# Performance work log

Hardware: AMD Instinct MI355X
Metric: run time of the kernel (lower is better)

## Reference

```python
import jax, jax.numpy as jnp
import numpy as np

N_NODES = 50000
N_EDGES = 800000
IN_FEAT = 128
HID = 128
OUT = 10
N_GRAPHS = 128
BN_EPS = 1e-5


def setup_inputs() -> dict:
    key = jax.random.key(0)
    ks = jax.random.split(key, 16)
    inp = {
        "n_feat": jax.random.normal(ks[0], (N_NODES, IN_FEAT), dtype=jnp.float32),
        "src": jax.random.randint(ks[1], (N_EDGES,), 0, N_NODES),
        "dst": jax.random.randint(ks[2], (N_EDGES,), 0, N_NODES),
        "graph_ids": jnp.sort(jax.random.randint(ks[3], (N_NODES,), 0, N_GRAPHS)),
        # GraphConv weights (DGL layout: weight [in, out], bias [out])
        "W1": jax.random.normal(ks[4], (IN_FEAT, HID), dtype=jnp.float32) / np.sqrt(IN_FEAT),
        "b1": jnp.zeros((HID,), dtype=jnp.float32),
        "W2": jax.random.normal(ks[5], (HID, HID), dtype=jnp.float32) / np.sqrt(HID),
        "b2": jnp.zeros((HID,), dtype=jnp.float32),
        # BatchNorm1d affine params
        "gamma": jnp.ones((HID,), dtype=jnp.float32),
        "beta": jnp.zeros((HID,), dtype=jnp.float32),
        # MLP head
        "fc1_w": jax.random.normal(ks[6], (HID, HID), dtype=jnp.float32) / np.sqrt(HID),
        "fc1_b": jnp.zeros((HID,), dtype=jnp.float32),
        "fc2_w": jax.random.normal(ks[7], (HID, OUT), dtype=jnp.float32) / np.sqrt(HID),
        "fc2_b": jnp.zeros((OUT,), dtype=jnp.float32),
    }
    return inp


def _graph_conv(x, W, b, src, dst, inv_sqrt_out, inv_sqrt_in):
    # DGL GraphConv, norm='both': h = D_in^{-1/2} A D_out^{-1/2} x W + b
    h = x * inv_sqrt_out[:, None]          # [N, d_in]
    h = h @ W                              # [N, d_out] (project before gather: fewer bytes moved)
    agg = jax.ops.segment_sum(h[src], dst, num_segments=N_NODES)  # gather + scatter-add
    return agg * inv_sqrt_in[:, None] + b


def reference(n_feat, src, dst, graph_ids, W1, b1, W2, b2, gamma, beta,
              fc1_w, fc1_b, fc2_w, fc2_b):
    ones_e = jnp.ones((N_EDGES,), dtype=jnp.float32)
    deg_out = jnp.clip(jax.ops.segment_sum(ones_e, src, num_segments=N_NODES), 1.0)
    deg_in = jnp.clip(jax.ops.segment_sum(ones_e, dst, num_segments=N_NODES), 1.0)
    inv_sqrt_out = jax.lax.rsqrt(deg_out)
    inv_sqrt_in = jax.lax.rsqrt(deg_in)

    x = jax.nn.relu(_graph_conv(n_feat, W1, b1, src, dst, inv_sqrt_out, inv_sqrt_in))
    # dropout is identity in eval mode
    x = jax.nn.relu(_graph_conv(x, W2, b2, src, dst, inv_sqrt_out, inv_sqrt_in))

    # SumPooling over graphs
    embedding = jax.ops.segment_sum(x, graph_ids, num_segments=N_GRAPHS)  # [B, HID]

    # BatchNorm1d (training-mode batch stats, biased variance like torch)
    mu = jnp.mean(embedding, axis=0)
    var = jnp.mean(jnp.square(embedding - mu), axis=0)
    h = gamma * (embedding - mu) * jax.lax.rsqrt(var + BN_EPS) + beta

    h = jax.nn.relu(h @ fc1_w + fc1_b)
    logits = h @ fc2_w + fc2_b
    return embedding, jax.nn.log_softmax(logits, axis=-1)
```

## Files before the change

kernel.cpp:

```cpp
#include <hip/hip_runtime.h>
#include <hip/hip_bf16.h>
#include <math.h>

#define N_NODES 50000
#define N_EDGES 800000
#define HID 128
#define N_GRAPHS 128
#define OUTC 10
#define BN_EPS 1e-5f

#define SCAN_B 256
#define N_SCAN_BLOCKS ((N_NODES + SCAN_B - 1) / SCAN_B)

#define POOL_CHUNK 32
#define N_POOL_BLOCKS ((N_NODES + POOL_CHUNK - 1) / POOL_CHUNK)

#define HB 80
#define HWORDS (N_NODES / 2)
#define HR_B 128
#define HR_BLOCKS ((HWORDS + HR_B - 1) / HR_B)

#define EPAD 8
#define E_SRC_CAP (N_EDGES + N_NODES * EPAD)

#define LDA 136

typedef short short8 __attribute__((ext_vector_type(8)));
typedef float floatx4 __attribute__((ext_vector_type(4)));

template <typename T, typename F>
__device__ inline T bitcast(F f) {
    union { F a; T b; } u;
    u.a = f;
    return u.b;
}

__global__ __launch_bounds__(1024) void hist_part_kernel(const int* __restrict__ src,
                                                         const int* __restrict__ dst,
                                                         unsigned int* __restrict__ part,
                                                         const float* __restrict__ W1,
                                                         const float* __restrict__ W2,
                                                         unsigned short* __restrict__ Wp) {
    if (blockIdx.x == 2 * HB) {
        for (int q = threadIdx.x; q < 4096; q += 1024) {
            int wi = q >> 11;
            const float* __restrict__ W = wi ? W2 : W1;
            int t2 = q & 2047;
            int tile = t2 >> 6, lane = t2 & 63;
            int kc = tile >> 3, nt = tile & 7;
            int n = lane & 15, quad = lane >> 4;
            unsigned short v[8];
#pragma unroll
            for (int j = 0; j < 8; j++) {
                int k = kc * 32 + quad * 8 + j;
                v[j] = __hip_bfloat16_raw(__float2bfloat16(W[k * HID + nt * 16 + n])).x;
            }
            *(uint4*)&Wp[(size_t)q * 8] = *(uint4*)v;
        }
        return;
    }
    __shared__ unsigned int h[HWORDS];
    for (int i = threadIdx.x; i < HWORDS; i += 1024) h[i] = 0;
    __syncthreads();
    int half = (blockIdx.x >= HB) ? 1 : 0;
    const int* __restrict__ idx = half ? dst : src;
    int b = blockIdx.x - half * HB;
    for (int e = b * 1024 + threadIdx.x; e < N_EDGES; e += HB * 1024) {
        int v = idx[e];
        atomicAdd(&h[v >> 1], 1u << ((v & 1) << 4));
    }
    __syncthreads();
    unsigned int* __restrict__ out = part + (size_t)blockIdx.x * HWORDS;
    for (int i = threadIdx.x; i < HWORDS; i += 1024) out[i] = h[i];
}

__global__ __launch_bounds__(HR_B) void hist_reduce_kernel(unsigned int* __restrict__ part,
                                                           int* __restrict__ cnt_in,
                                                           float* __restrict__ inv_out,
                                                           float* __restrict__ inv_in,
                                                           int* __restrict__ bsum) {
    int w = blockIdx.x * HR_B + threadIdx.x;
    int padsum = 0;
    if (w < HWORDS) {
        unsigned int s = 0, d = 0;
        for (int b = 0; b < HB; b++) {
            s += part[(size_t)b * HWORDS + w];
            unsigned int c = part[(size_t)(b + HB) * HWORDS + w];
            part[(size_t)(b + HB) * HWORDS + w] = d;
            d += c;
        }
        int i0 = w * 2, i1 = i0 + 1;
        int so0 = (int)(s & 0xFFFFu), so1 = (int)(s >> 16);
        int di0 = (int)(d & 0xFFFFu), di1 = (int)(d >> 16);
        cnt_in[i0] = di0;
        cnt_in[i1] = di1;
        inv_out[i0] = rsqrtf(fmaxf((float)so0, 1.0f));
        inv_out[i1] = rsqrtf(fmaxf((float)so1, 1.0f));
        inv_in[i0] = rsqrtf(fmaxf((float)di0, 1.0f));
        inv_in[i1] = rsqrtf(fmaxf((float)di1, 1.0f));
        padsum = ((di0 + EPAD - 1) & ~(EPAD - 1)) + ((di1 + EPAD - 1) & ~(EPAD - 1));
    }
    __shared__ int red[HR_B];
    red[threadIdx.x] = padsum;
    __syncthreads();
    for (int o = HR_B / 2; o > 0; o >>= 1) {
        if (threadIdx.x < o) red[threadIdx.x] += red[threadIdx.x + o];
        __syncthreads();
    }
    if (threadIdx.x == 0) bsum[blockIdx.x] = red[0];
}

__global__ void scan_bsum_kernel(const int* __restrict__ bsum, int* __restrict__ boff) {
    __shared__ int part[SCAN_B];
    int t = threadIdx.x;
    int v = (t < N_SCAN_BLOCKS) ? bsum[t] : 0;
    part[t] = v;
    __syncthreads();
    for (int off = 1; off < SCAN_B; off <<= 1) {
        int u = (t >= off) ? part[t - off] : 0;
        __syncthreads();
        part[t] += u;
        __syncthreads();
    }
    boff[t] = part[t] - v;
}

__global__ void scan_write_kernel(const int* __restrict__ cnt, const int* __restrict__ boff,
                                  int* __restrict__ row_ptr, int* __restrict__ edge_src) {
    __shared__ int part[SCAN_B];
    int t = threadIdx.x;
    int i = blockIdx.x * SCAN_B + t;
    int raw = (i < N_NODES) ? cnt[i] : 0;
    int v = (raw + EPAD - 1) & ~(EPAD - 1);
    part[t] = v;
    __syncthreads();
    for (int off = 1; off < SCAN_B; off <<= 1) {
        int u = (t >= off) ? part[t - off] : 0;
        __syncthreads();
        part[t] += u;
        __syncthreads();
    }
    if (i < N_NODES) {
        int ex = part[t] - v + boff[blockIdx.x];
        row_ptr[i] = ex;
        for (int p = ex + raw; p < ex + v; p++) edge_src[p] = N_NODES;
        if (i == N_NODES - 1) row_ptr[N_NODES] = ex + v;
    }
}

__global__ __launch_bounds__(1024) void csr_fill_kernel(const int* __restrict__ src,
                                                        const int* __restrict__ dst,
                                                        const unsigned int* __restrict__ part,
                                                        const int* __restrict__ row_ptr,
                                                        int* __restrict__ edge_src) {
    __shared__ unsigned int loc[HWORDS];
    int b = blockIdx.x;
    const unsigned int* __restrict__ off = part + (size_t)(b + HB) * HWORDS;
    for (int i = threadIdx.x; i < HWORDS; i += 1024) loc[i] = off[i];
    __syncthreads();
    for (int e = b * 1024 + threadIdx.x; e < N_EDGES; e += HB * 1024) {
        int d = dst[e];
        unsigned int old = atomicAdd(&loc[d >> 1], 1u << ((d & 1) << 4));
        int local = (d & 1) ? (int)(old >> 16) : (int)(old & 0xFFFFu);
        edge_src[row_ptr[d] + local] = src[e];
    }
}

__global__ __launch_bounds__(256) void matmul_kernel(const float* __restrict__ X,
                                                     const float* __restrict__ scale,
                                                     const unsigned short* __restrict__ Wp,
                                                     __hip_bfloat16* __restrict__ Y) {
    __shared__ unsigned short xs[64 * LDA];
    int tid = threadIdx.x;
    int row0 = blockIdx.x * 64;

    for (int j = 0; j < 8; j++) {
        int idx4 = j * 256 + tid;
        int r = idx4 >> 5;
        int col = (idx4 & 31) * 4;
        int rg = row0 + r;
        float4 v = make_float4(0.f, 0.f, 0.f, 0.f);
        if (rg < N_NODES) {
            v = *(const float4*)&X[(size_t)rg * HID + col];
            float sc = scale[rg];
            v.x *= sc; v.y *= sc; v.z *= sc; v.w *= sc;
        }
        unsigned short o[4];
        o[0] = __hip_bfloat16_raw(__float2bfloat16(v.x)).x;
        o[1] = __hip_bfloat16_raw(__float2bfloat16(v.y)).x;
        o[2] = __hip_bfloat16_raw(__float2bfloat16(v.z)).x;
        o[3] = __hip_bfloat16_raw(__float2bfloat16(v.w)).x;
        *(ushort4*)&xs[r * LDA + col] = *(ushort4*)o;
    }
    __syncthreads();

    int wave = tid >> 6, lane = tid & 63;
    int m = lane & 15, quad = lane >> 4;
    int rowl = wave * 16;

    short8 a[4];
#pragma unroll
    for (int kc = 0; kc < 4; kc++)
        a[kc] = bitcast<short8>(*(const uint4*)&xs[(rowl + m) * LDA + kc * 32 + quad * 8]);

    floatx4 acc[8];
#pragma unroll
    for (int nt = 0; nt < 8; nt++) acc[nt] = (floatx4){0.f, 0.f, 0.f, 0.f};

#pragma unroll
    for (int nt = 0; nt < 8; nt++) {
#pragma unroll
        for (int kc = 0; kc < 4; kc++) {
            short8 bfr = bitcast<short8>(
                *(const uint4*)&Wp[((size_t)(kc * 8 + nt) * 64 + lane) * 8]);
            acc[nt] = __builtin_amdgcn_mfma_f32_16x16x32_bf16(a[kc], bfr, acc[nt], 0, 0, 0);
        }
    }

#pragma unroll
    for (int nt = 0; nt < 8; nt++) {
#pragma unroll
        for (int i = 0; i < 4; i++) {
            int rg = row0 + rowl + quad * 4 + i;
            if (rg < N_NODES + 1) {
                Y[(size_t)rg * HID + nt * 16 + m] = __float2bfloat16(acc[nt][i]);
            }
        }
    }
}

__global__ __launch_bounds__(256) void agg_kernel(const __hip_bfloat16* __restrict__ Y,
                                                  const int* __restrict__ edge_src,
                                                  const int* __restrict__ row_ptr,
                                                  const float* __restrict__ inv_in,
                                                  const float* __restrict__ bias,
                                                  float* __restrict__ Xout) {
    const uint4* __restrict__ Yq = (const uint4*)Y;
    int wave = threadIdx.x >> 6;
    int lane = threadIdx.x & 63;
    int n = blockIdx.x * 4 + wave;
    if (n >= N_NODES) return;
    int beg = row_ptr[n], end = row_ptr[n + 1];
    int esub = lane >> 4;
    int f16  = lane & 15;
    float acc[8] = {};
    for (int base = beg; base < end; base += 64) {
        int mm = min(64, end - base);
        int idx = (lane < mm) ? edge_src[base + lane] : N_NODES;
        for (int j = 0; j < mm; j += 8) {
            int s0 = __shfl(idx, j + esub);
            int s1 = __shfl(idx, j + 4 + esub);
            uint4 u0 = Yq[s0 * (HID / 8) + f16];
            uint4 u1 = Yq[s1 * (HID / 8) + f16];
            acc[0] += __uint_as_float(u0.x << 16); acc[1] += __uint_as_float(u0.x & 0xFFFF0000u);
            acc[2] += __uint_as_float(u0.y << 16); acc[3] += __uint_as_float(u0.y & 0xFFFF0000u);
            acc[4] += __uint_as_float(u0.z << 16); acc[5] += __uint_as_float(u0.z & 0xFFFF0000u);
            acc[6] += __uint_as_float(u0.w << 16); acc[7] += __uint_as_float(u0.w & 0xFFFF0000u);
            acc[0] += __uint_as_float(u1.x << 16); acc[1] += __uint_as_float(u1.x & 0xFFFF0000u);
            acc[2] += __uint_as_float(u1.y << 16); acc[3] += __uint_as_float(u1.y & 0xFFFF0000u);
            acc[4] += __uint_as_float(u1.z << 16); acc[5] += __uint_as_float(u1.z & 0xFFFF0000u);
            acc[6] += __uint_as_float(u1.w << 16); acc[7] += __uint_as_float(u1.w & 0xFFFF0000u);
        }
    }
#pragma unroll
    for (int i = 0; i < 8; i++) {
        acc[i] += __shfl_xor(acc[i], 16);
        acc[i] += __shfl_xor(acc[i], 32);
    }
    if (lane < 16) {
        float si = inv_in[n];
        int f0 = f16 * 8;
        float4 b0 = *(const float4*)&bias[f0];
        float4 b1 = *(const float4*)&bias[f0 + 4];
        float4 o0, o1;
        o0.x = fmaxf(acc[0] * si + b0.x, 0.f);
        o0.y = fmaxf(acc[1] * si + b0.y, 0.f);
        o0.z = fmaxf(acc[2] * si + b0.z, 0.f);
        o0.w = fmaxf(acc[3] * si + b0.w, 0.f);
        o1.x = fmaxf(acc[4] * si + b1.x, 0.f);
        o1.y = fmaxf(acc[5] * si + b1.y, 0.f);
        o1.z = fmaxf(acc[6] * si + b1.z, 0.f);
        o1.w = fmaxf(acc[7] * si + b1.w, 0.f);
        *(float4*)&Xout[(size_t)n * HID + f0] = o0;
        *(float4*)&Xout[(size_t)n * HID + f0 + 4] = o1;
    }
}

__global__ __launch_bounds__(64) void pool_kernel(const float* __restrict__ X,
                                                  const int* __restrict__ gid,
                                                  float* __restrict__ emb) {
    int lane = threadIdx.x;
    int n0 = blockIdx.x * POOL_CHUNK;
    int n1 = min(n0 + POOL_CHUNK, N_NODES);
    if (n0 >= N_NODES) return;
    int g_cur = gid[n0];
    float ax = 0.f, ay = 0.f;
    for (int n = n0; n < n1; n++) {
        int g = gid[n];
        if (g != g_cur) {
            atomicAdd(&emb[g_cur * HID + lane * 2], ax);
            atomicAdd(&emb[g_cur * HID + lane * 2 + 1], ay);
            ax = 0.f; ay = 0.f;
            g_cur = g;
        }
        float2 v = *(const float2*)&X[(size_t)n * HID + lane * 2];
        ax += v.x;
        ay += v.y;
    }
    atomicAdd(&emb[g_cur * HID + lane * 2], ax);
    atomicAdd(&emb[g_cur * HID + lane * 2 + 1], ay);
}

__global__ __launch_bounds__(128) void head_fused_kernel(const float* __restrict__ emb,
                                                         const float* __restrict__ gamma,
                                                         const float* __restrict__ beta,
                                                         const float* __restrict__ fc1_w,
                                                         const float* __restrict__ fc1_b,
                                                         const float* __restrict__ fc2_w,
                                                         const float* __restrict__ fc2_b,
                                                         float* __restrict__ out) {
    int r = blockIdx.x, f = threadIdx.x;
    float s = 0.f;
    for (int row = 0; row < N_GRAPHS; row++) s += emb[row * HID + f];
    float mu = s * (1.f / N_GRAPHS);
    float v = 0.f;
    for (int row = 0; row < N_GRAPHS; row++) {
        float d = emb[row * HID + f] - mu;
        v += d * d;
    }
    v *= (1.f / N_GRAPHS);
    float sc = gamma[f] * rsqrtf(v + BN_EPS);
    float sh = beta[f] - mu * sc;

    __shared__ float xr[HID];
    xr[f] = emb[r * HID + f] * sc + sh;
    __syncthreads();
    float acc = fc1_b[f];
    for (int k = 0; k < HID; k++) acc += xr[k] * fc1_w[k * HID + f];
    __shared__ float hr[HID];
    hr[f] = fmaxf(acc, 0.f);
    __syncthreads();

    __shared__ float logits[OUTC];
    __shared__ float mstat[2];
    if (f < OUTC) {
        float a = fc2_b[f];
        for (int k = 0; k < HID; k++) a += hr[k] * fc2_w[k * OUTC + f];
        logits[f] = a;
    }
    __syncthreads();
    if (f == 0) {
        float m = logits[0];
        for (int o = 1; o < OUTC; o++) m = fmaxf(m, logits[o]);
        float sum = 0.f;
        for (int o = 0; o < OUTC; o++) sum += expf(logits[o] - m);
        mstat[0] = m;
        mstat[1] = logf(sum);
    }
    __syncthreads();
    if (f < OUTC) out[r * OUTC + f] = logits[f] - mstat[0] - mstat[1];
}

extern "C" void kernel_launch(void* const* d_in, const int* in_sizes, int n_in,
                              void* d_out, int out_size, void* d_ws, size_t ws_size,
                              hipStream_t stream) {
    const float* n_feat = (const float*)d_in[0];
    const int*   src    = (const int*)d_in[1];
    const int*   dst    = (const int*)d_in[2];
    const int*   gid    = (const int*)d_in[3];
    const float* W1     = (const float*)d_in[4];
    const float* b1     = (const float*)d_in[5];
    const float* W2     = (const float*)d_in[6];
    const float* b2     = (const float*)d_in[7];
    const float* gamma  = (const float*)d_in[8];
    const float* beta   = (const float*)d_in[9];
    const float* fc1_w  = (const float*)d_in[10];
    const float* fc1_b  = (const float*)d_in[11];
    const float* fc2_w  = (const float*)d_in[12];
    const float* fc2_b  = (const float*)d_in[13];

    char* wsb = (char*)d_ws;
    size_t off = 0;
    auto alloc = [&](size_t bytes) -> void* {
        void* p = wsb + off;
        off += (bytes + 255) & ~(size_t)255;
        return p;
    };
    int*   cnt_in  = (int*)alloc((size_t)N_NODES * 4);
    int*   row_ptr = (int*)alloc((size_t)(N_NODES + 1) * 4);
    int*   e_src   = (int*)alloc((size_t)E_SRC_CAP * 4);
    float* inv_out = (float*)alloc((size_t)N_NODES * 4);
    float* inv_in  = (float*)alloc((size_t)N_NODES * 4);
    void*  ybuf    = alloc((size_t)2 * HB * HWORDS * 4);
    float* X       = (float*)alloc((size_t)N_NODES * HID * 4);
    unsigned short* Wp = (unsigned short*)alloc((size_t)2 * 32 * 64 * 8 * 2);
    int*   bsum    = (int*)alloc((size_t)SCAN_B * 4);
    int*   boff    = (int*)alloc((size_t)SCAN_B * 4);

    unsigned int*   part = (unsigned int*)ybuf;
    __hip_bfloat16* Y    = (__hip_bfloat16*)ybuf;

    float* emb_out = (float*)d_out;
    float* lsm_out = emb_out + N_GRAPHS * HID;

    hipMemsetAsync(emb_out, 0, (size_t)N_GRAPHS * HID * 4, stream);

    hist_part_kernel<<<2 * HB + 1, 1024, 0, stream>>>(src, dst, part, W1, W2, Wp);
    hist_reduce_kernel<<<HR_BLOCKS, HR_B, 0, stream>>>(part, cnt_in, inv_out, inv_in, bsum);
    scan_bsum_kernel<<<1, SCAN_B, 0, stream>>>(bsum, boff);
    scan_write_kernel<<<N_SCAN_BLOCKS, SCAN_B, 0, stream>>>(cnt_in, boff, row_ptr, e_src);
    csr_fill_kernel<<<HB, 1024, 0, stream>>>(src, dst, part, row_ptr, e_src);

    matmul_kernel<<<(N_NODES + 64) / 64, 256, 0, stream>>>(n_feat, inv_out, Wp, Y);
    agg_kernel<<<(N_NODES + 3) / 4, 256, 0, stream>>>(Y, e_src, row_ptr, inv_in, b1, X);
    matmul_kernel<<<(N_NODES + 64) / 64, 256, 0, stream>>>(X, inv_out, Wp + (size_t)32 * 64 * 8, Y);
    agg_kernel<<<(N_NODES + 3) / 4, 256, 0, stream>>>(Y, e_src, row_ptr, inv_in, b2, X);

    pool_kernel<<<N_POOL_BLOCKS, 64, 0, stream>>>(X, gid, emb_out);
    head_fused_kernel<<<N_GRAPHS, HID, 0, stream>>>(emb_out, gamma, beta, fc1_w, fc1_b,
                                                    fc2_w, fc2_b, lsm_out);
}
```

Measured before the change: 254.6 us.

## Fuse CSR-build kernels via grid barriers, emit bf16 layer-1 output, fuse pool+head

Merges the histogram, reduce, scan and CSR-fill kernels into one persistent kernel that separates its phases with atomic-counter grid barriers. It also merges the pooling and head kernels the same way, and drops the memset of the embedding. The first aggregation now applies the out-degree scale and writes bf16, so the second matmul reads half the bytes and skips conversion. This removes several launch gaps and one fp32 round trip. In exchange it relies on all blocks being co-resident for the spin barriers, which risks deadlock if they are not.

```diff
diff --git a/kernel.cpp b/kernel.cpp
--- a/kernel.cpp
+++ b/kernel.cpp
@@ -9,21 +9,18 @@
 #define OUTC 10
 #define BN_EPS 1e-5f
 
-#define SCAN_B 256
-#define N_SCAN_BLOCKS ((N_NODES + SCAN_B - 1) / SCAN_B)
-
-#define POOL_CHUNK 32
-#define N_POOL_BLOCKS ((N_NODES + POOL_CHUNK - 1) / POOL_CHUNK)
-
 #define HB 80
 #define HWORDS (N_NODES / 2)
 #define HR_B 128
-#define HR_BLOCKS ((HWORDS + HR_B - 1) / HR_B)
+#define NPRE 196
 
 #define EPAD 8
 #define E_SRC_CAP (N_EDGES + N_NODES * EPAD)
 
 #define LDA 136
+
+#define PH_BLOCKS 256
+#define PH_NODES ((N_NODES + PH_BLOCKS - 1) / PH_BLOCKS)
 
 typedef short short8 __attribute__((ext_vector_type(8)));
 typedef float floatx4 __attribute__((ext_vector_type(4)));
@@ -35,14 +32,56 @@
     return u.b;
 }
 
-__global__ __launch_bounds__(1024) void hist_part_kernel(const int* __restrict__ src,
-                                                         const int* __restrict__ dst,
-                                                         unsigned int* __restrict__ part,
-                                                         const float* __restrict__ W1,
-                                                         const float* __restrict__ W2,
-                                                         unsigned short* __restrict__ Wp) {
-    if (blockIdx.x == 2 * HB) {
-        for (int q = threadIdx.x; q < 4096; q += 1024) {
+__device__ inline unsigned short f2bf(float x) {
+    return __hip_bfloat16_raw(__float2bfloat16(x)).x;
+}
+
+__device__ inline void grid_sync(unsigned int* ctr, unsigned int nblk, bool wait) {
+    __syncthreads();
+    if (threadIdx.x == 0) {
+        __hip_atomic_fetch_add(ctr, 1u, __ATOMIC_RELEASE, __HIP_MEMORY_SCOPE_AGENT);
+        if (wait) {
+            while (__hip_atomic_load(ctr, __ATOMIC_RELAXED, __HIP_MEMORY_SCOPE_AGENT) < nblk)
+                __builtin_amdgcn_s_sleep(2);
+        }
+    }
+    __syncthreads();
+    if (wait) __threadfence();
+}
+
+__global__ __launch_bounds__(1024) void pre_kernel(const int* __restrict__ src,
+                                                   const int* __restrict__ dst,
+                                                   unsigned int* __restrict__ part,
+                                                   const float* __restrict__ W1,
+                                                   const float* __restrict__ W2,
+                                                   unsigned short* __restrict__ Wp,
+                                                   float* __restrict__ inv_out,
+                                                   float* __restrict__ inv_in,
+                                                   int* __restrict__ row_ptr,
+                                                   int* __restrict__ edge_src,
+                                                   int* __restrict__ bsum,
+                                                   float* __restrict__ emb,
+                                                   unsigned int* __restrict__ ctr) {
+    __shared__ unsigned int big[HWORDS];
+    __shared__ int cnts[2 * HR_B];
+    __shared__ int red[HR_B];
+    int b = blockIdx.x, t = threadIdx.x;
+
+    if (b < 2 * HB) {
+        for (int i = t; i < HWORDS; i += 1024) big[i] = 0;
+        __syncthreads();
+        int half = (b >= HB) ? 1 : 0;
+        const int* __restrict__ idx = half ? dst : src;
+        int bb = b - half * HB;
+        for (int e = bb * 1024 + t; e < N_EDGES; e += HB * 1024) {
+            int v = idx[e];
+            atomicAdd(&big[v >> 1], 1u << ((v & 1) << 4));
+        }
+        __syncthreads();
+        unsigned int* __restrict__ out = part + (size_t)b * HWORDS;
+        for (int i = t; i < HWORDS; i += 1024) out[i] = big[i];
+    } else if (b == 2 * HB) {
+        for (int q = t; q < 4096; q += 1024) {
             int wi = q >> 11;
             const float* __restrict__ W = wi ? W2 : W1;
             int t2 = q & 2047;
@@ -53,116 +92,130 @@
 #pragma unroll
             for (int j = 0; j < 8; j++) {
                 int k = kc * 32 + quad * 8 + j;
-                v[j] = __hip_bfloat16_raw(__float2bfloat16(W[k * HID + nt * 16 + n])).x;
+                v[j] = f2bf(W[k * HID + nt * 16 + n]);
             }
             *(uint4*)&Wp[(size_t)q * 8] = *(uint4*)v;
         }
-        return;
-    }
-    __shared__ unsigned int h[HWORDS];
-    for (int i = threadIdx.x; i < HWORDS; i += 1024) h[i] = 0;
-    __syncthreads();
-    int half = (blockIdx.x >= HB) ? 1 : 0;
-    const int* __restrict__ idx = half ? dst : src;
-    int b = blockIdx.x - half * HB;
-    for (int e = b * 1024 + threadIdx.x; e < N_EDGES; e += HB * 1024) {
-        int v = idx[e];
-        atomicAdd(&h[v >> 1], 1u << ((v & 1) << 4));
-    }
-    __syncthreads();
-    unsigned int* __restrict__ out = part + (size_t)blockIdx.x * HWORDS;
-    for (int i = threadIdx.x; i < HWORDS; i += 1024) out[i] = h[i];
-}
-
-__global__ __launch_bounds__(HR_B) void hist_reduce_kernel(unsigned int* __restrict__ part,
-                                                           int* __restrict__ cnt_in,
-                                                           float* __restrict__ inv_out,
-                                                           float* __restrict__ inv_in,
-                                                           int* __restrict__ bsum) {
-    int w = blockIdx.x * HR_B + threadIdx.x;
+    } else if (b == 2 * HB + 1) {
+        for (int i = t; i < N_GRAPHS * HID; i += 1024) emb[i] = 0.f;
+    }
+    grid_sync(ctr + 0, NPRE, true);
+
     int padsum = 0;
-    if (w < HWORDS) {
-        unsigned int s = 0, d = 0;
-        for (int b = 0; b < HB; b++) {
-            s += part[(size_t)b * HWORDS + w];
-            unsigned int c = part[(size_t)(b + HB) * HWORDS + w];
-            part[(size_t)(b + HB) * HWORDS + w] = d;
-            d += c;
-        }
-        int i0 = w * 2, i1 = i0 + 1;
-        int so0 = (int)(s & 0xFFFFu), so1 = (int)(s >> 16);
-        int di0 = (int)(d & 0xFFFFu), di1 = (int)(d >> 16);
-        cnt_in[i0] = di0;
-        cnt_in[i1] = di1;
-        inv_out[i0] = rsqrtf(fmaxf((float)so0, 1.0f));
-        inv_out[i1] = rsqrtf(fmaxf((float)so1, 1.0f));
-        inv_in[i0] = rsqrtf(fmaxf((float)di0, 1.0f));
-        inv_in[i1] = rsqrtf(fmaxf((float)di1, 1.0f));
-        padsum = ((di0 + EPAD - 1) & ~(EPAD - 1)) + ((di1 + EPAD - 1) & ~(EPAD - 1));
-    }
-    __shared__ int red[HR_B];
-    red[threadIdx.x] = padsum;
+    if (t < HR_B) {
+        int w = b * HR_B + t;
+        int di0 = 0, di1 = 0;
+        if (w < HWORDS) {
+            unsigned int s = 0, d = 0;
+#pragma unroll 10
+            for (int bb = 0; bb < HB; bb++) {
+                s += part[(size_t)bb * HWORDS + w];
+                unsigned int c = part[(size_t)(bb + HB) * HWORDS + w];
+                part[(size_t)(bb + HB) * HWORDS + w] = d;
+                d += c;
+            }
+            int i0 = w * 2, i1 = i0 + 1;
+            int so0 = (int)(s & 0xFFFFu), so1 = (int)(s >> 16);
+            di0 = (int)(d & 0xFFFFu);
+            di1 = (int)(d >> 16);
+            inv_out[i0] = rsqrtf(fmaxf((float)so0, 1.0f));
+            inv_out[i1] = rsqrtf(fmaxf((float)so1, 1.0f));
+            inv_in[i0] = rsqrtf(fmaxf((float)di0, 1.0f));
+            inv_in[i1] = rsqrtf(fmaxf((float)di1, 1.0f));
+            padsum = ((di0 + EPAD - 1) & ~(EPAD - 1)) + ((di1 + EPAD - 1) & ~(EPAD - 1));
+        }
+        cnts[2 * t] = di0;
+        cnts[2 * t + 1] = di1;
+        red[t] = padsum;
+    }
     __syncthreads();
     for (int o = HR_B / 2; o > 0; o >>= 1) {
-        if (threadIdx.x < o) red[threadIdx.x] += red[threadIdx.x + o];
-        __syncthreads();
-    }
-    if (threadIdx.x == 0) bsum[blockIdx.x] = red[0];
-}
-
-__global__ void scan_bsum_kernel(const int* __restrict__ bsum, int* __restrict__ boff) {
-    __shared__ int part[SCAN_B];
-    int t = threadIdx.x;
-    int v = (t < N_SCAN_BLOCKS) ? bsum[t] : 0;
-    part[t] = v;
-    __syncthreads();
-    for (int off = 1; off < SCAN_B; off <<= 1) {
-        int u = (t >= off) ? part[t - off] : 0;
-        __syncthreads();
-        part[t] += u;
-        __syncthreads();
-    }
-    boff[t] = part[t] - v;
-}
-
-__global__ void scan_write_kernel(const int* __restrict__ cnt, const int* __restrict__ boff,
-                                  int* __restrict__ row_ptr, int* __restrict__ edge_src) {
-    __shared__ int part[SCAN_B];
-    int t = threadIdx.x;
-    int i = blockIdx.x * SCAN_B + t;
-    int raw = (i < N_NODES) ? cnt[i] : 0;
+        if (t < o) red[t] += red[t + o];
+        __syncthreads();
+    }
+    if (t == 0) bsum[b] = red[0];
+    grid_sync(ctr + 1, NPRE, true);
+
+    int* sb = (int*)big;
+    int* sc = (int*)big + 256;
+    if (t < 256) sb[t] = (t < NPRE) ? bsum[t] : 0;
+    __syncthreads();
+    for (int off = 1; off < 256; off <<= 1) {
+        int u = (t < 256 && t >= off) ? sb[t - off] : 0;
+        __syncthreads();
+        if (t < 256) sb[t] += u;
+        __syncthreads();
+    }
+    int boff = sb[b] - red[0];
+    int raw = (t < 256) ? cnts[t] : 0;
     int v = (raw + EPAD - 1) & ~(EPAD - 1);
-    part[t] = v;
-    __syncthreads();
-    for (int off = 1; off < SCAN_B; off <<= 1) {
-        int u = (t >= off) ? part[t - off] : 0;
-        __syncthreads();
-        part[t] += u;
-        __syncthreads();
-    }
-    if (i < N_NODES) {
-        int ex = part[t] - v + boff[blockIdx.x];
-        row_ptr[i] = ex;
-        for (int p = ex + raw; p < ex + v; p++) edge_src[p] = N_NODES;
-        if (i == N_NODES - 1) row_ptr[N_NODES] = ex + v;
-    }
-}
-
-__global__ __launch_bounds__(1024) void csr_fill_kernel(const int* __restrict__ src,
-                                                        const int* __restrict__ dst,
-                                                        const unsigned int* __restrict__ part,
-                                                        const int* __restrict__ row_ptr,
-                                                        int* __restrict__ edge_src) {
-    __shared__ unsigned int loc[HWORDS];
-    int b = blockIdx.x;
-    const unsigned int* __restrict__ off = part + (size_t)(b + HB) * HWORDS;
-    for (int i = threadIdx.x; i < HWORDS; i += 1024) loc[i] = off[i];
-    __syncthreads();
-    for (int e = b * 1024 + threadIdx.x; e < N_EDGES; e += HB * 1024) {
+    if (t < 256) sc[t] = v;
+    __syncthreads();
+    for (int off = 1; off < 256; off <<= 1) {
+        int u = (t < 256 && t >= off) ? sc[t - off] : 0;
+        __syncthreads();
+        if (t < 256) sc[t] += u;
+        __syncthreads();
+    }
+    if (t < 256) {
+        int i = b * 256 + t;
+        if (i < N_NODES) {
+            int ex = sc[t] - v + boff;
+            row_ptr[i] = ex;
+            for (int p = ex + raw; p < ex + v; p++) edge_src[p] = N_NODES;
+            if (i == N_NODES - 1) row_ptr[N_NODES] = ex + v;
+        }
+    }
+    grid_sync(ctr + 2, NPRE, b < HB);
+    if (b >= HB) return;
+
+    const unsigned int* __restrict__ off3 = part + (size_t)(b + HB) * HWORDS;
+    for (int i = t; i < HWORDS; i += 1024) big[i] = off3[i];
+    __syncthreads();
+    for (int e = b * 1024 + t; e < N_EDGES; e += HB * 1024) {
         int d = dst[e];
-        unsigned int old = atomicAdd(&loc[d >> 1], 1u << ((d & 1) << 4));
+        unsigned int old = atomicAdd(&big[d >> 1], 1u << ((d & 1) << 4));
         int local = (d & 1) ? (int)(old >> 16) : (int)(old & 0xFFFFu);
         edge_src[row_ptr[d] + local] = src[e];
+    }
+}
+
+__device__ inline void mm_tail(const unsigned short* __restrict__ xs,
+                               const unsigned short* __restrict__ Wp,
+                               __hip_bfloat16* __restrict__ Y, int row0) {
+    int tid = threadIdx.x;
+    int wave = tid >> 6, lane = tid & 63;
+    int m = lane & 15, quad = lane >> 4;
+    int rowl = wave * 16;
+
+    short8 a[4];
+#pragma unroll
+    for (int kc = 0; kc < 4; kc++)
+        a[kc] = bitcast<short8>(*(const uint4*)&xs[(rowl + m) * LDA + kc * 32 + quad * 8]);
+
+    floatx4 acc[8];
+#pragma unroll
+    for (int nt = 0; nt < 8; nt++) acc[nt] = (floatx4){0.f, 0.f, 0.f, 0.f};
+
+#pragma unroll
+    for (int nt = 0; nt < 8; nt++) {
+#pragma unroll
+        for (int kc = 0; kc < 4; kc++) {
+            short8 bfr = bitcast<short8>(
+                *(const uint4*)&Wp[((size_t)(kc * 8 + nt) * 64 + lane) * 8]);
+            acc[nt] = __builtin_amdgcn_mfma_f32_16x16x32_bf16(a[kc], bfr, acc[nt], 0, 0, 0);
+        }
+    }
+
+#pragma unroll
+    for (int nt = 0; nt < 8; nt++) {
+#pragma unroll
+        for (int i = 0; i < 4; i++) {
+            int rg = row0 + rowl + quad * 4 + i;
+            if (rg < N_NODES + 1) {
+                Y[(size_t)rg * HID + nt * 16 + m] = __float2bfloat16(acc[nt][i]);
+            }
+        }
     }
 }
 
@@ -173,7 +226,6 @@
     __shared__ unsigned short xs[64 * LDA];
     int tid = threadIdx.x;
     int row0 = blockIdx.x * 64;
-
     for (int j = 0; j < 8; j++) {
         int idx4 = j * 256 + tid;
         int r = idx4 >> 5;
@@ -186,55 +238,40 @@
             v.x *= sc; v.y *= sc; v.z *= sc; v.w *= sc;
         }
         unsigned short o[4];
-        o[0] = __hip_bfloat16_raw(__float2bfloat16(v.x)).x;
-        o[1] = __hip_bfloat16_raw(__float2bfloat16(v.y)).x;
-        o[2] = __hip_bfloat16_raw(__float2bfloat16(v.z)).x;
-        o[3] = __hip_bfloat16_raw(__float2bfloat16(v.w)).x;
+        o[0] = f2bf(v.x); o[1] = f2bf(v.y); o[2] = f2bf(v.z); o[3] = f2bf(v.w);
         *(ushort4*)&xs[r * LDA + col] = *(ushort4*)o;
     }
     __syncthreads();
-
-    int wave = tid >> 6, lane = tid & 63;
-    int m = lane & 15, quad = lane >> 4;
-    int rowl = wave * 16;
-
-    short8 a[4];
-#pragma unroll
-    for (int kc = 0; kc < 4; kc++)
-        a[kc] = bitcast<short8>(*(const uint4*)&xs[(rowl + m) * LDA + kc * 32 + quad * 8]);
-
-    floatx4 acc[8];
-#pragma unroll
-    for (int nt = 0; nt < 8; nt++) acc[nt] = (floatx4){0.f, 0.f, 0.f, 0.f};
-
-#pragma unroll
-    for (int nt = 0; nt < 8; nt++) {
-#pragma unroll
-        for (int kc = 0; kc < 4; kc++) {
-            short8 bfr = bitcast<short8>(
-                *(const uint4*)&Wp[((size_t)(kc * 8 + nt) * 64 + lane) * 8]);
-            acc[nt] = __builtin_amdgcn_mfma_f32_16x16x32_bf16(a[kc], bfr, acc[nt], 0, 0, 0);
-        }
-    }
-
-#pragma unroll
-    for (int nt = 0; nt < 8; nt++) {
-#pragma unroll
-        for (int i = 0; i < 4; i++) {
-            int rg = row0 + rowl + quad * 4 + i;
-            if (rg < N_NODES + 1) {
-                Y[(size_t)rg * HID + nt * 16 + m] = __float2bfloat16(acc[nt][i]);
-            }
-        }
-    }
-}
-
-__global__ __launch_bounds__(256) void agg_kernel(const __hip_bfloat16* __restrict__ Y,
-                                                  const int* __restrict__ edge_src,
-                                                  const int* __restrict__ row_ptr,
-                                                  const float* __restrict__ inv_in,
-                                                  const float* __restrict__ bias,
-                                                  float* __restrict__ Xout) {
+    mm_tail(xs, Wp, Y, row0);
+}
+
+__global__ __launch_bounds__(256) void matmul_bf16_kernel(const __hip_bfloat16* __restrict__ Xb,
+                                                          const unsigned short* __restrict__ Wp,
+                                                          __hip_bfloat16* __restrict__ Y) {
+    __shared__ unsigned short xs[64 * LDA];
+    int tid = threadIdx.x;
+    int row0 = blockIdx.x * 64;
+    for (int j = 0; j < 4; j++) {
+        int idx8 = j * 256 + tid;
+        int r = idx8 >> 4;
+        int c = (idx8 & 15) * 8;
+        int rg = row0 + r;
+        uint4 v = make_uint4(0u, 0u, 0u, 0u);
+        if (rg < N_NODES) v = *(const uint4*)&Xb[(size_t)rg * HID + c];
+        *(uint4*)&xs[r * LDA + c] = v;
+    }
+    __syncthreads();
+    mm_tail(xs, Wp, Y, row0);
+}
+
+template <bool BF16OUT>
+__global__ __launch_bounds__(256) void agg_kernel_t(const __hip_bfloat16* __restrict__ Y,
+                                                    const int* __restrict__ edge_src,
+                                                    const int* __restrict__ row_ptr,
+                                                    const float* __restrict__ inv_in,
+                                                    const float* __restrict__ inv_out,
+                                                    const float* __restrict__ bias,
+                                                    void* __restrict__ Xout) {
     const uint4* __restrict__ Yq = (const uint4*)Y;
     int wave = threadIdx.x >> 6;
     int lane = threadIdx.x & 63;
@@ -242,7 +279,7 @@
     if (n >= N_NODES) return;
     int beg = row_ptr[n], end = row_ptr[n + 1];
     int esub = lane >> 4;
-    int f16  = lane & 15;
+    int f16 = lane & 15;
     float acc[8] = {};
     for (int base = beg; base < end; base += 64) {
         int mm = min(64, end - base);
@@ -272,90 +309,97 @@
         int f0 = f16 * 8;
         float4 b0 = *(const float4*)&bias[f0];
         float4 b1 = *(const float4*)&bias[f0 + 4];
-        float4 o0, o1;
-        o0.x = fmaxf(acc[0] * si + b0.x, 0.f);
-        o0.y = fmaxf(acc[1] * si + b0.y, 0.f);
-        o0.z = fmaxf(acc[2] * si + b0.z, 0.f);
-        o0.w = fmaxf(acc[3] * si + b0.w, 0.f);
-        o1.x = fmaxf(acc[4] * si + b1.x, 0.f);
-        o1.y = fmaxf(acc[5] * si + b1.y, 0.f);
-        o1.z = fmaxf(acc[6] * si + b1.z, 0.f);
-        o1.w = fmaxf(acc[7] * si + b1.w, 0.f);
-        *(float4*)&Xout[(size_t)n * HID + f0] = o0;
-        *(float4*)&Xout[(size_t)n * HID + f0 + 4] = o1;
-    }
-}
-
-__global__ __launch_bounds__(64) void pool_kernel(const float* __restrict__ X,
-                                                  const int* __restrict__ gid,
-                                                  float* __restrict__ emb) {
-    int lane = threadIdx.x;
-    int n0 = blockIdx.x * POOL_CHUNK;
-    int n1 = min(n0 + POOL_CHUNK, N_NODES);
-    if (n0 >= N_NODES) return;
-    int g_cur = gid[n0];
-    float ax = 0.f, ay = 0.f;
-    for (int n = n0; n < n1; n++) {
-        int g = gid[n];
-        if (g != g_cur) {
-            atomicAdd(&emb[g_cur * HID + lane * 2], ax);
-            atomicAdd(&emb[g_cur * HID + lane * 2 + 1], ay);
-            ax = 0.f; ay = 0.f;
-            g_cur = g;
-        }
-        float2 v = *(const float2*)&X[(size_t)n * HID + lane * 2];
-        ax += v.x;
-        ay += v.y;
-    }
-    atomicAdd(&emb[g_cur * HID + lane * 2], ax);
-    atomicAdd(&emb[g_cur * HID + lane * 2 + 1], ay);
-}
-
-__global__ __launch_bounds__(128) void head_fused_kernel(const float* __restrict__ emb,
-                                                         const float* __restrict__ gamma,
-                                                         const float* __restrict__ beta,
-                                                         const float* __restrict__ fc1_w,
-                                                         const float* __restrict__ fc1_b,
-                                                         const float* __restrict__ fc2_w,
-                                                         const float* __restrict__ fc2_b,
-                                                         float* __restrict__ out) {
-    int r = blockIdx.x, f = threadIdx.x;
+        float o[8];
+        o[0] = fmaxf(acc[0] * si + b0.x, 0.f);
+        o[1] = fmaxf(acc[1] * si + b0.y, 0.f);
+        o[2] = fmaxf(acc[2] * si + b0.z, 0.f);
+        o[3] = fmaxf(acc[3] * si + b0.w, 0.f);
+        o[4] = fmaxf(acc[4] * si + b1.x, 0.f);
+        o[5] = fmaxf(acc[5] * si + b1.y, 0.f);
+        o[6] = fmaxf(acc[6] * si + b1.z, 0.f);
+        o[7] = fmaxf(acc[7] * si + b1.w, 0.f);
+        if constexpr (BF16OUT) {
+            float so = inv_out[n];
+            unsigned short u[8];
+#pragma unroll
+            for (int i = 0; i < 8; i++) u[i] = f2bf(o[i] * so);
+            *(uint4*)&((__hip_bfloat16*)Xout)[(size_t)n * HID + f0] = *(uint4*)u;
+        } else {
+            float* Xf = (float*)Xout;
+            *(float4*)&Xf[(size_t)n * HID + f0] = make_float4(o[0], o[1], o[2], o[3]);
+            *(float4*)&Xf[(size_t)n * HID + f0 + 4] = make_float4(o[4], o[5], o[6], o[7]);
+        }
+    }
+}
+
+__global__ __launch_bounds__(128) void poolhead_kernel(const float* __restrict__ X,
+                                                       const int* __restrict__ gid,
+                                                       const float* __restrict__ gamma,
+                                                       const float* __restrict__ beta,
+                                                       const float* __restrict__ fc1_w,
+                                                       const float* __restrict__ fc1_b,
+                                                       const float* __restrict__ fc2_w,
+                                                       const float* __restrict__ fc2_b,
+                                                       float* __restrict__ emb,
+                                                       float* __restrict__ out,
+                                                       unsigned int* __restrict__ ctr) {
+    int b = blockIdx.x, f = threadIdx.x;
+    int n0 = b * PH_NODES;
+    int n1 = min(n0 + PH_NODES, N_NODES);
+    if (n0 < N_NODES) {
+        int g_cur = gid[n0];
+        float a = 0.f;
+        for (int n = n0; n < n1; n++) {
+            int g = gid[n];
+            if (g != g_cur) {
+                atomicAdd(&emb[g_cur * HID + f], a);
+                a = 0.f;
+                g_cur = g;
+            }
+            a += X[(size_t)n * HID + f];
+        }
+        atomicAdd(&emb[g_cur * HID + f], a);
+    }
+    grid_sync(ctr, PH_BLOCKS, b < N_GRAPHS);
+    if (b >= N_GRAPHS) return;
+
+    int r = b;
     float s = 0.f;
     for (int row = 0; row < N_GRAPHS; row++) s += emb[row * HID + f];
     float mu = s * (1.f / N_GRAPHS);
-    float v = 0.f;
+    float var = 0.f;
     for (int row = 0; row < N_GRAPHS; row++) {
-        float d = emb[row * HID + f] - mu;
-        v += d * d;
-    }
-    v *= (1.f / N_GRAPHS);
-    float sc = gamma[f] * rsqrtf(v + BN_EPS);
-    float sh = beta[f] - mu * sc;
+        float d2 = emb[row * HID + f] - mu;
+        var += d2 * d2;
+    }
+    var *= (1.f / N_GRAPHS);
+    float scb = gamma[f] * rsqrtf(var + BN_EPS);
+    float sh = beta[f] - mu * scb;
 
     __shared__ float xr[HID];
-    xr[f] = emb[r * HID + f] * sc + sh;
+    __shared__ float hr[HID];
+    xr[f] = emb[r * HID + f] * scb + sh;
     __syncthreads();
     float acc = fc1_b[f];
     for (int k = 0; k < HID; k++) acc += xr[k] * fc1_w[k * HID + f];
-    __shared__ float hr[HID];
     hr[f] = fmaxf(acc, 0.f);
     __syncthreads();
 
     __shared__ float logits[OUTC];
     __shared__ float mstat[2];
     if (f < OUTC) {
-        float a = fc2_b[f];
-        for (int k = 0; k < HID; k++) a += hr[k] * fc2_w[k * OUTC + f];
-        logits[f] = a;
+        float a2 = fc2_b[f];
+        for (int k = 0; k < HID; k++) a2 += hr[k] * fc2_w[k * OUTC + f];
+        logits[f] = a2;
     }
     __syncthreads();
     if (f == 0) {
         float m = logits[0];
         for (int o = 1; o < OUTC; o++) m = fmaxf(m, logits[o]);
-        float sum = 0.f;
-        for (int o = 0; o < OUTC; o++) sum += expf(logits[o] - m);
+        float su = 0.f;
+        for (int o = 0; o < OUTC; o++) su += expf(logits[o] - m);
         mstat[0] = m;
-        mstat[1] = logf(sum);
+        mstat[1] = logf(su);
     }
     __syncthreads();
     if (f < OUTC) out[r * OUTC + f] = logits[f] - mstat[0] - mstat[1];
@@ -386,16 +430,16 @@
         off += (bytes + 255) & ~(size_t)255;
         return p;
     };
-    int*   cnt_in  = (int*)alloc((size_t)N_NODES * 4);
     int*   row_ptr = (int*)alloc((size_t)(N_NODES + 1) * 4);
     int*   e_src   = (int*)alloc((size_t)E_SRC_CAP * 4);
     float* inv_out = (float*)alloc((size_t)N_NODES * 4);
     float* inv_in  = (float*)alloc((size_t)N_NODES * 4);
     void*  ybuf    = alloc((size_t)2 * HB * HWORDS * 4);
     float* X       = (float*)alloc((size_t)N_NODES * HID * 4);
+    __hip_bfloat16* X1b = (__hip_bfloat16*)alloc((size_t)N_NODES * HID * 2);
     unsigned short* Wp = (unsigned short*)alloc((size_t)2 * 32 * 64 * 8 * 2);
-    int*   bsum    = (int*)alloc((size_t)SCAN_B * 4);
-    int*   boff    = (int*)alloc((size_t)SCAN_B * 4);
+    int*   bsum    = (int*)alloc((size_t)256 * 4);
+    unsigned int* ctrs = (unsigned int*)alloc(256);
 
     unsigned int*   part = (unsigned int*)ybuf;
     __hip_bfloat16* Y    = (__hip_bfloat16*)ybuf;
@@ -403,20 +447,18 @@
     float* emb_out = (float*)d_out;
     float* lsm_out = emb_out + N_GRAPHS * HID;
 
-    hipMemsetAsync(emb_out, 0, (size_t)N_GRAPHS * HID * 4, stream);
-
-    hist_part_kernel<<<2 * HB + 1, 1024, 0, stream>>>(src, dst, part, W1, W2, Wp);
-    hist_reduce_kernel<<<HR_BLOCKS, HR_B, 0, stream>>>(part, cnt_in, inv_out, inv_in, bsum);
-    scan_bsum_kernel<<<1, SCAN_B, 0, stream>>>(bsum, boff);
-    scan_write_kernel<<<N_SCAN_BLOCKS, SCAN_B, 0, stream>>>(cnt_in, boff, row_ptr, e_src);
-    csr_fill_kernel<<<HB, 1024, 0, stream>>>(src, dst, part, row_ptr, e_src);
+    hipMemsetAsync(ctrs, 0, 256, stream);
+
+    pre_kernel<<<NPRE, 1024, 0, stream>>>(src, dst, part, W1, W2, Wp, inv_out, inv_in,
+                                          row_ptr, e_src, bsum, emb_out, ctrs + 0);
 
     matmul_kernel<<<(N_NODES + 64) / 64, 256, 0, stream>>>(n_feat, inv_out, Wp, Y);
-    agg_kernel<<<(N_NODES + 3) / 4, 256, 0, stream>>>(Y, e_src, row_ptr, inv_in, b1, X);
-    matmul_kernel<<<(N_NODES + 64) / 64, 256, 0, stream>>>(X, inv_out, Wp + (size_t)32 * 64 * 8, Y);
-    agg_kernel<<<(N_NODES + 3) / 4, 256, 0, stream>>>(Y, e_src, row_ptr, inv_in, b2, X);
-
-    pool_kernel<<<N_POOL_BLOCKS, 64, 0, stream>>>(X, gid, emb_out);
-    head_fused_kernel<<<N_GRAPHS, HID, 0, stream>>>(emb_out, gamma, beta, fc1_w, fc1_b,
-                                                    fc2_w, fc2_b, lsm_out);
-}
+    agg_kernel_t<true><<<(N_NODES + 3) / 4, 256, 0, stream>>>(Y, e_src, row_ptr, inv_in,
+                                                              inv_out, b1, X1b);
+    matmul_bf16_kernel<<<(N_NODES + 64) / 64, 256, 0, stream>>>(X1b, Wp + (size_t)32 * 64 * 8, Y);
+    agg_kernel_t<false><<<(N_NODES + 3) / 4, 256, 0, stream>>>(Y, e_src, row_ptr, inv_in,
+                                                               nullptr, b2, X);
+
+    poolhead_kernel<<<PH_BLOCKS, 128, 0, stream>>>(X, gid, gamma, beta, fc1_w, fc1_b,
+                                                   fc2_w, fc2_b, emb_out, lsm_out, ctrs + 16);
+}
```

Measured after the change: 440.5 us. 1.73x slower.

## Emit pre-scaled bf16 layer-1 output from aggregation and merge scan kernels

Applied to the files above, without the earlier changes.

The first aggregation kernel now applies the out-degree scale and writes its activations as bf16, so the second matmul reads half the bytes and skips the scale-and-convert step. The separate block-sum scan kernel is folded into the scan-write kernel, with every block redundantly scanning the block sums, which removes one launch. The cost is an extra bf16 buffer and repeated small scans in each block.

```diff
diff --git a/kernel.cpp b/kernel.cpp
--- a/kernel.cpp
+++ b/kernel.cpp
@@ -33,6 +33,10 @@
     union { F a; T b; } u;
     u.a = f;
     return u.b;
+}
+
+__device__ inline unsigned short f2bf(float x) {
+    return __hip_bfloat16_raw(__float2bfloat16(x)).x;
 }
 
 __global__ __launch_bounds__(1024) void hist_part_kernel(const int* __restrict__ src,
@@ -53,7 +57,7 @@
 #pragma unroll
             for (int j = 0; j < 8; j++) {
                 int k = kc * 32 + quad * 8 + j;
-                v[j] = __hip_bfloat16_raw(__float2bfloat16(W[k * HID + nt * 16 + n])).x;
+                v[j] = f2bf(W[k * HID + nt * 16 + n]);
             }
             *(uint4*)&Wp[(size_t)q * 8] = *(uint4*)v;
         }
@@ -110,10 +114,24 @@
     if (threadIdx.x == 0) bsum[blockIdx.x] = red[0];
 }
 
-__global__ void scan_bsum_kernel(const int* __restrict__ bsum, int* __restrict__ boff) {
+__global__ void scan_write_kernel(const int* __restrict__ cnt, const int* __restrict__ bsum,
+                                  int* __restrict__ row_ptr, int* __restrict__ edge_src) {
+    __shared__ int sb[SCAN_B];
     __shared__ int part[SCAN_B];
     int t = threadIdx.x;
-    int v = (t < N_SCAN_BLOCKS) ? bsum[t] : 0;
+    sb[t] = (t < N_SCAN_BLOCKS) ? bsum[t] : 0;
+    __syncthreads();
+    for (int off = 1; off < SCAN_B; off <<= 1) {
+        int u = (t >= off) ? sb[t - off] : 0;
+        __syncthreads();
+        sb[t] += u;
+        __syncthreads();
+    }
+    int boff = (blockIdx.x == 0) ? 0 : sb[blockIdx.x - 1];
+
+    int i = blockIdx.x * SCAN_B + t;
+    int raw = (i < N_NODES) ? cnt[i] : 0;
+    int v = (raw + EPAD - 1) & ~(EPAD - 1);
     part[t] = v;
     __syncthreads();
     for (int off = 1; off < SCAN_B; off <<= 1) {
@@ -122,26 +140,8 @@
         part[t] += u;
         __syncthreads();
     }
-    boff[t] = part[t] - v;
-}
-
-__global__ void scan_write_kernel(const int* __restrict__ cnt, const int* __restrict__ boff,
-                                  int* __restrict__ row_ptr, int* __restrict__ edge_src) {
-    __shared__ int part[SCAN_B];
-    int t = threadIdx.x;
-    int i = blockIdx.x * SCAN_B + t;
-    int raw = (i < N_NODES) ? cnt[i] : 0;
-    int v = (raw + EPAD - 1) & ~(EPAD - 1);
-    part[t] = v;
-    __syncthreads();
-    for (int off = 1; off < SCAN_B; off <<= 1) {
-        int u = (t >= off) ? part[t - off] : 0;
-        __syncthreads();
-        part[t] += u;
-        __syncthreads();
-    }
     if (i < N_NODES) {
-        int ex = part[t] - v + boff[blockIdx.x];
+        int ex = part[t] - v + boff;
         row_ptr[i] = ex;
         for (int p = ex + raw; p < ex + v; p++) edge_src[p] = N_NODES;
         if (i == N_NODES - 1) row_ptr[N_NODES] = ex + v;
@@ -166,6 +166,45 @@
     }
 }
 
+__device__ inline void mm_tail(const unsigned short* __restrict__ xs,
+                               const unsigned short* __restrict__ Wp,
+                               __hip_bfloat16* __restrict__ Y, int row0) {
+    int tid = threadIdx.x;
+    int wave = tid >> 6, lane = tid & 63;
+    int m = lane & 15, quad = lane >> 4;
+    int rowl = wave * 16;
+
+    short8 a[4];
+#pragma unroll
+    for (int kc = 0; kc < 4; kc++)
+        a[kc] = bitcast<short8>(*(const uint4*)&xs[(rowl + m) * LDA + kc * 32 + quad * 8]);
+
+    floatx4 acc[8];
+#pragma unroll
+    for (int nt = 0; nt < 8; nt++) acc[nt] = (floatx4){0.f, 0.f, 0.f, 0.f};
+
+#pragma unroll
+    for (int nt = 0; nt < 8; nt++) {
+#pragma unroll
+        for (int kc = 0; kc < 4; kc++) {
+            short8 bfr = bitcast<short8>(
+                *(const uint4*)&Wp[((size_t)(kc * 8 + nt) * 64 + lane) * 8]);
+            acc[nt] = __builtin_amdgcn_mfma_f32_16x16x32_bf16(a[kc], bfr, acc[nt], 0, 0, 0);
+        }
+    }
+
+#pragma unroll
+    for (int nt = 0; nt < 8; nt++) {
+#pragma unroll
+        for (int i = 0; i < 4; i++) {
+            int rg = row0 + rowl + quad * 4 + i;
+            if (rg < N_NODES + 1) {
+                Y[(size_t)rg * HID + nt * 16 + m] = __float2bfloat16(acc[nt][i]);
+            }
+        }
+    }
+}
+
 __global__ __launch_bounds__(256) void matmul_kernel(const float* __restrict__ X,
                                                      const float* __restrict__ scale,
                                                      const unsigned short* __restrict__ Wp,
@@ -173,7 +212,6 @@
     __shared__ unsigned short xs[64 * LDA];
     int tid = threadIdx.x;
     int row0 = blockIdx.x * 64;
-
     for (int j = 0; j < 8; j++) {
         int idx4 = j * 256 + tid;
         int r = idx4 >> 5;
@@ -186,55 +224,40 @@
             v.x *= sc; v.y *= sc; v.z *= sc; v.w *= sc;
         }
         unsigned short o[4];
-        o[0] = __hip_bfloat16_raw(__float2bfloat16(v.x)).x;
-        o[1] = __hip_bfloat16_raw(__float2bfloat16(v.y)).x;
-        o[2] = __hip_bfloat16_raw(__float2bfloat16(v.z)).x;
-        o[3] = __hip_bfloat16_raw(__float2bfloat16(v.w)).x;
+        o[0] = f2bf(v.x); o[1] = f2bf(v.y); o[2] = f2bf(v.z); o[3] = f2bf(v.w);
         *(ushort4*)&xs[r * LDA + col] = *(ushort4*)o;
     }
     __syncthreads();
-
-    int wave = tid >> 6, lane = tid & 63;
-    int m = lane & 15, quad = lane >> 4;
-    int rowl = wave * 16;
-
-    short8 a[4];
-#pragma unroll
-    for (int kc = 0; kc < 4; kc++)
-        a[kc] = bitcast<short8>(*(const uint4*)&xs[(rowl + m) * LDA + kc * 32 + quad * 8]);
-
-    floatx4 acc[8];
-#pragma unroll
-    for (int nt = 0; nt < 8; nt++) acc[nt] = (floatx4){0.f, 0.f, 0.f, 0.f};
-
-#pragma unroll
-    for (int nt = 0; nt < 8; nt++) {
-#pragma unroll
-        for (int kc = 0; kc < 4; kc++) {
-            short8 bfr = bitcast<short8>(
-                *(const uint4*)&Wp[((size_t)(kc * 8 + nt) * 64 + lane) * 8]);
-            acc[nt] = __builtin_amdgcn_mfma_f32_16x16x32_bf16(a[kc], bfr, acc[nt], 0, 0, 0);
-        }
-    }
-
-#pragma unroll
-    for (int nt = 0; nt < 8; nt++) {
-#pragma unroll
-        for (int i = 0; i < 4; i++) {
-            int rg = row0 + rowl + quad * 4 + i;
-            if (rg < N_NODES + 1) {
-                Y[(size_t)rg * HID + nt * 16 + m] = __float2bfloat16(acc[nt][i]);
-            }
-        }
-    }
-}
-
-__global__ __launch_bounds__(256) void agg_kernel(const __hip_bfloat16* __restrict__ Y,
-                                                  const int* __restrict__ edge_src,
-                                                  const int* __restrict__ row_ptr,
-                                                  const float* __restrict__ inv_in,
-                                                  const float* __restrict__ bias,
-                                                  float* __restrict__ Xout) {
+    mm_tail(xs, Wp, Y, row0);
+}
+
+__global__ __launch_bounds__(256) void matmul_bf16_kernel(const __hip_bfloat16* __restrict__ Xb,
+                                                          const unsigned short* __restrict__ Wp,
+                                                          __hip_bfloat16* __restrict__ Y) {
+    __shared__ unsigned short xs[64 * LDA];
+    int tid = threadIdx.x;
+    int row0 = blockIdx.x * 64;
+    for (int j = 0; j < 4; j++) {
+        int idx8 = j * 256 + tid;
+        int r = idx8 >> 4;
+        int c = (idx8 & 15) * 8;
+        int rg = row0 + r;
+        uint4 v = make_uint4(0u, 0u, 0u, 0u);
+        if (rg < N_NODES) v = *(const uint4*)&Xb[(size_t)rg * HID + c];
+        *(uint4*)&xs[r * LDA + c] = v;
+    }
+    __syncthreads();
+    mm_tail(xs, Wp, Y, row0);
+}
+
+template <bool BF16OUT>
+__global__ __launch_bounds__(256) void agg_kernel_t(const __hip_bfloat16* __restrict__ Y,
+                                                    const int* __restrict__ edge_src,
+                                                    const int* __restrict__ row_ptr,
+                                                    const float* __restrict__ inv_in,
+                                                    const float* __restrict__ inv_out,
+                                                    const float* __restrict__ bias,
+                                                    void* __restrict__ Xout) {
     const uint4* __restrict__ Yq = (const uint4*)Y;
     int wave = threadIdx.x >> 6;
     int lane = threadIdx.x & 63;
@@ -272,17 +295,26 @@
         int f0 = f16 * 8;
         float4 b0 = *(const float4*)&bias[f0];
         float4 b1 = *(const float4*)&bias[f0 + 4];
-        float4 o0, o1;
-        o0.x = fmaxf(acc[0] * si + b0.x, 0.f);
-        o0.y = fmaxf(acc[1] * si + b0.y, 0.f);
-        o0.z = fmaxf(acc[2] * si + b0.z, 0.f);
-        o0.w = fmaxf(acc[3] * si + b0.w, 0.f);
-        o1.x = fmaxf(acc[4] * si + b1.x, 0.f);
-        o1.y = fmaxf(acc[5] * si + b1.y, 0.f);
-        o1.z = fmaxf(acc[6] * si + b1.z, 0.f);
-        o1.w = fmaxf(acc[7] * si + b1.w, 0.f);
-        *(float4*)&Xout[(size_t)n * HID + f0] = o0;
-        *(float4*)&Xout[(size_t)n * HID + f0 + 4] = o1;
+        float o[8];
+        o[0] = fmaxf(acc[0] * si + b0.x, 0.f);
+        o[1] = fmaxf(acc[1] * si + b0.y, 0.f);
+        o[2] = fmaxf(acc[2] * si + b0.z, 0.f);
+        o[3] = fmaxf(acc[3] * si + b0.w, 0.f);
+        o[4] = fmaxf(acc[4] * si + b1.x, 0.f);
+        o[5] = fmaxf(acc[5] * si + b1.y, 0.f);
+        o[6] = fmaxf(acc[6] * si + b1.z, 0.f);
+        o[7] = fmaxf(acc[7] * si + b1.w, 0.f);
+        if constexpr (BF16OUT) {
+            float so = inv_out[n];
+            unsigned short u[8];
+#pragma unroll
+            for (int i = 0; i < 8; i++) u[i] = f2bf(o[i] * so);
+            *(uint4*)&((__hip_bfloat16*)Xout)[(size_t)n * HID + f0] = *(uint4*)u;
+        } else {
+            float* Xf = (float*)Xout;
+            *(float4*)&Xf[(size_t)n * HID + f0] = make_float4(o[0], o[1], o[2], o[3]);
+            *(float4*)&Xf[(size_t)n * HID + f0 + 4] = make_float4(o[4], o[5], o[6], o[7]);
+        }
     }
 }
 
@@ -393,9 +425,9 @@
     float* inv_in  = (float*)alloc((size_t)N_NODES * 4);
     void*  ybuf    = alloc((size_t)2 * HB * HWORDS * 4);
     float* X       = (float*)alloc((size_t)N_NODES * HID * 4);
+    __hip_bfloat16* X1b = (__hip_bfloat16*)alloc((size_t)N_NODES * HID * 2);
     unsigned short* Wp = (unsigned short*)alloc((size_t)2 * 32 * 64 * 8 * 2);
     int*   bsum    = (int*)alloc((size_t)SCAN_B * 4);
-    int*   boff    = (int*)alloc((size_t)SCAN_B * 4);
 
     unsigned int*   part = (unsigned int*)ybuf;
     __hip_bfloat16* Y    = (__hip_bfloat16*)ybuf;
@@ -407,14 +439,15 @@
 
     hist_part_kernel<<<2 * HB + 1, 1024, 0, stream>>>(src, dst, part, W1, W2, Wp);
     hist_reduce_kernel<<<HR_BLOCKS, HR_B, 0, stream>>>(part, cnt_in, inv_out, inv_in, bsum);
-    scan_bsum_kernel<<<1, SCAN_B, 0, stream>>>(bsum, boff);
-    scan_write_kernel<<<N_SCAN_BLOCKS, SCAN_B, 0, stream>>>(cnt_in, boff, row_ptr, e_src);
+    scan_write_kernel<<<N_SCAN_BLOCKS, SCAN_B, 0, stream>>>(cnt_in, bsum, row_ptr, e_src);
     csr_fill_kernel<<<HB, 1024, 0, stream>>>(src, dst, part, row_ptr, e_src);
 
     matmul_kernel<<<(N_NODES + 64) / 64, 256, 0, stream>>>(n_feat, inv_out, Wp, Y);
-    agg_kernel<<<(N_NODES + 3) / 4, 256, 0, stream>>>(Y, e_src, row_ptr, inv_in, b1, X);
-    matmul_kernel<<<(N_NODES + 64) / 64, 256, 0, stream>>>(X, inv_out, Wp + (size_t)32 * 64 * 8, Y);
-    agg_kernel<<<(N_NODES + 3) / 4, 256, 0, stream>>>(Y, e_src, row_ptr, inv_in, b2, X);
+    agg_kernel_t<true><<<(N_NODES + 3) / 4, 256, 0, stream>>>(Y, e_src, row_ptr, inv_in,
+                                                              inv_out, b1, X1b);
+    matmul_bf16_kernel<<<(N_NODES + 64) / 64, 256, 0, stream>>>(X1b, Wp + (size_t)32 * 64 * 8, Y);
+    agg_kernel_t<false><<<(N_NODES + 3) / 4, 256, 0, stream>>>(Y, e_src, row_ptr, inv_in,
+                                                               nullptr, b2, X);
 
     pool_kernel<<<N_POOL_BLOCKS, 64, 0, stream>>>(X, gid, emb_out);
     head_fused_kernel<<<N_GRAPHS, HID, 0, stream>>>(emb_out, gamma, beta, fc1_w, fc1_b,
```

After: 256.3 us. About the same (+0.7%).
